# Performance work log

Measured on AMD Instinct MI355X. Metric: run time of the kernel, lower is better.

The kernel has to match this reference:

```python
import jax, jax.numpy as jnp
import numpy as np
from jax import lax


def get_grid(h, w):
    # normalized [-1,1] grid, channel 0 = x, channel 1 = y, shape [1,h,w,2]
    gx, gy = jnp.meshgrid(jnp.linspace(-1.0, 1.0, w), jnp.linspace(-1.0, 1.0, h))
    return jnp.stack([gx, gy], axis=-1)[None].astype(jnp.float32)


def gaussian_kernel(k, sigma=1.0):
    c = jnp.arange(k, dtype=jnp.float32) - (k - 1) / 2.0
    g = jnp.exp(-(c ** 2) / (2.0 * sigma ** 2))
    k2 = jnp.outer(g, g)
    return k2 / k2.sum()


def resize_bilinear(x, H, W):
    # x: [B,C,h,w]; torch F.interpolate(mode='bilinear', align_corners=False)
    B, C, h, w = x.shape
    def coords(n_out, n_in):
        c = (jnp.arange(n_out, dtype=jnp.float32) + 0.5) * (n_in / n_out) - 0.5
        c = jnp.clip(c, 0.0, n_in - 1.0)
        lo = jnp.floor(c).astype(jnp.int32)
        hi = jnp.minimum(lo + 1, n_in - 1)
        return lo, hi, c - lo.astype(jnp.float32)
    y0, y1, wy = coords(H, h)
    x0, x1, wx = coords(W, w)
    r = x[:, :, y0, :] * (1.0 - wy)[None, None, :, None] + x[:, :, y1, :] * wy[None, None, :, None]
    return r[:, :, :, x0] * (1.0 - wx) + r[:, :, :, x1] * wx


def _forward(src_grid, kernel, src_grid_base, tgt_grid, niter):
    B = src_grid.shape[0]
    H, W = tgt_grid.shape[1], tgt_grid.shape[2]
    ks = kernel.shape[-1]
    HW = H * W
    # forward displacement, resampled to target resolution, in pixel units
    dsrc = (src_grid - src_grid_base).transpose(0, 3, 1, 2)        # [B,2,Hs,Ws]
    dsrc = resize_bilinear(dsrc, H, W)                              # [B,2,H,W]
    dx = dsrc[:, 0].reshape(B, HW) * (W / 2.0)
    dy = dsrc[:, 1].reshape(B, HW) * (H / 2.0)
    xg = (jnp.arange(HW) % W).astype(jnp.float32)
    yg = (jnp.arange(HW) // W).astype(jnp.float32)
    xi = jnp.round(xg[None] + dx).astype(jnp.int32)
    yi = jnp.round(yg[None] + dy).astype(jnp.int32)
    oob = (xi < 0) | (yi < 0) | (xi > W - 1) | (yi > H - 1)
    field = jnp.where(oob, -1, yi * W + xi) + 1   # index 0 = trash slot
    # sort + dedup: duplicates are redirected to the trash slot
    order = jnp.argsort(field, axis=1)            # stable
    sf = jnp.take_along_axis(field, order, axis=1)
    keep = jnp.concatenate([jnp.ones((B, 1), bool), sf[:, 1:] != sf[:, :-1]], axis=1)
    sf = sf * keep
    inv_order = jnp.argsort(order, axis=1)
    field = jnp.take_along_axis(sf, inv_order, axis=1)
    # scatter inverse displacement (unique indices except trash slot 0)
    z = jnp.zeros((B, 1), dtype=dx.dtype)
    dxp = jnp.concatenate([z, dx], axis=1)
    dyp = jnp.concatenate([z, dy], axis=1)
    fieldp = jnp.concatenate([jnp.zeros((B, 1), field.dtype), field], axis=1)
    bidx = jnp.arange(B)[:, None]
    inv_dx = jnp.zeros_like(dxp).at[bidx, fieldp].set(-dxp)[:, 1:].reshape(B, H, W)
    inv_dy = jnp.zeros_like(dyp).at[bidx, fieldp].set(-dyp)[:, 1:].reshape(B, H, W)
    mask = (jnp.zeros_like(dxp).at[bidx, fieldp].set(1.0)[:, 1:].reshape(B, H, W)) > 0.5
    # pad so hole-fill never reads outside
    p = niter + 1
    inv_dx = jnp.pad(inv_dx, ((0, 0), (p, p), (p, p)))
    inv_dy = jnp.pad(inv_dy, ((0, 0), (p, p), (p, p)))
    mask = jnp.pad(mask, ((0, 0), (p, p), (p, p)))
    pd = ks // 2
    k4 = kernel.reshape(1, 1, ks, ks)
    def conv(x):
        return lax.conv_general_dilated(x[:, None], k4, (1, 1), [(pd, pd), (pd, pd)])[:, 0]
    # hole-fill: dilate mask by 4-neighborhood, fill with gaussian-weighted avg
    for _ in range(niter):
        nb = (jnp.pad(mask, ((0, 0), (1, 0), (0, 0)))[:, :-1]
              | jnp.pad(mask, ((0, 0), (0, 1), (0, 0)))[:, 1:]
              | jnp.pad(mask, ((0, 0), (0, 0), (1, 0)))[:, :, :-1]
              | jnp.pad(mask, ((0, 0), (0, 0), (0, 1)))[:, :, 1:])
        new_mask = (~mask) & nb
        new_dx = conv(inv_dx)
        new_dy = conv(inv_dy)
        new_sum = conv(mask.astype(inv_dx.dtype))
        denom = jnp.where(new_mask, new_sum, 1.0)  # safe: new_sum>0 where new_mask
        inv_dx = jnp.where(new_mask, new_dx / denom, inv_dx)
        inv_dy = jnp.where(new_mask, new_dy / denom, inv_dy)
        mask = mask | new_mask
    # erode: drop pixels with any unmasked 4-neighbor (outside counts as masked)
    for _ in range(niter):
        full = (jnp.pad(mask, ((0, 0), (1, 0), (0, 0)), constant_values=True)[:, :-1]
                & jnp.pad(mask, ((0, 0), (0, 1), (0, 0)), constant_values=True)[:, 1:]
                & jnp.pad(mask, ((0, 0), (0, 0), (1, 0)), constant_values=True)[:, :, :-1]
                & jnp.pad(mask, ((0, 0), (0, 0), (0, 1)), constant_values=True)[:, :, 1:])
        mask = mask & full
    inv_dx = jnp.where(mask, inv_dx, 2.0 * W)
    inv_dy = jnp.where(mask, inv_dy, 2.0 * H)
    inv_dx = inv_dx[:, p:-p, p:-p]
    inv_dy = inv_dy[:, p:-p, p:-p]
    dtgt = jnp.stack([inv_dx * (2.0 / W), inv_dy * (2.0 / H)], axis=3)
    return tgt_grid + dtgt


def setup_inputs() -> dict:
    key = jax.random.key(0)
    B, Hs, Ws, H, W = 8, 256, 256, 512, 512
    base = get_grid(Hs, Ws)
    src_grid = base + 0.05 * jax.random.normal(key, (B, Hs, Ws, 2), jnp.float32)
    return {
        "src_grid": src_grid,
        "kernel": gaussian_kernel(3),
        "src_grid_base": base,
        "tgt_grid": get_grid(H, W),
        "niter": 5,
    }


def reference(src_grid, kernel, src_grid_base, tgt_grid, niter):
    return _forward(src_grid, kernel, src_grid_base, tgt_grid, niter)
```

## Files before the change

### kernel.cpp

```cpp
#include <hip/hip_runtime.h>
#include <hip/hip_fp16.h>

typedef unsigned long long u64;
typedef unsigned int u32;
typedef float float4a __attribute__((ext_vector_type(4), aligned(4)));

#define B_    8
#define HS_   256
#define WS_   256
#define H_    512
#define W_    512
#define HW_   (H_ * W_)
#define TO_Y  16
#define WR    36
#define WCOLS 276
#define VR    26
#define VCOLS 266
#define VSTR  267
#define OW    9
#define NBAND 32
#define NBKT  64
#define INFW  0xFFFFFFFFu
#define CAPB  8192

__device__ __forceinline__ void bilin_disp(const float* __restrict__ src,
                                           const float* __restrict__ base,
                                           int b, int y, int x,
                                           float& dx, float& dy) {
#pragma clang fp contract(off)
    float cy = ((float)y + 0.5f) * 0.5f - 0.5f;
    cy = fminf(fmaxf(cy, 0.0f), 255.0f);
    int   y0 = (int)floorf(cy);
    int   y1 = min(y0 + 1, HS_ - 1);
    float wy = cy - (float)y0;

    float cx = ((float)x + 0.5f) * 0.5f - 0.5f;
    cx = fminf(fmaxf(cx, 0.0f), 255.0f);
    int   x0 = (int)floorf(cx);
    float wx = cx - (float)x0;

    float omy = 1.0f - wy;
    float wA, wB;
    int xs;
    if (x0 >= WS_ - 1) { xs = WS_ - 2; wA = 0.0f; wB = 1.0f; }
    else               { xs = x0;      wA = 1.0f - wx; wB = wx; }

    const float4a* S0 = (const float4a*)(src  + ((b * HS_ + y0) * WS_ + xs) * 2);
    const float4a* S1 = (const float4a*)(src  + ((b * HS_ + y1) * WS_ + xs) * 2);
    const float4a* B0 = (const float4a*)(base + (y0 * WS_ + xs) * 2);
    const float4a* B1 = (const float4a*)(base + (y1 * WS_ + xs) * 2);
    float4a s0 = *S0, s1 = *S1, b0 = *B0, b1 = *B1;

    float a00x = s0.x - b0.x, a00y = s0.y - b0.y;
    float a01x = s0.z - b0.z, a01y = s0.w - b0.w;
    float a10x = s1.x - b1.x, a10y = s1.y - b1.y;
    float a11x = s1.z - b1.z, a11y = s1.w - b1.w;

    float r0x = a00x * omy + a10x * wy;
    float r0y = a00y * omy + a10y * wy;
    float r1x = a01x * omy + a11x * wy;
    float r1y = a01y * omy + a11y * wy;
    dx = (r0x * wA + r1x * wB) * 256.0f;
    dy = (r0y * wA + r1y * wB) * 256.0f;
}

__device__ __forceinline__ u32 pack16(float x, float y) {
    __half hx = __float2half_rn(x), hy = __float2half_rn(y);
    return ((u32)__half_as_ushort(hy) << 16) | (u32)__half_as_ushort(hx);
}
__device__ __forceinline__ float2 unpack16(u32 p) {
    float2 f;
    f.x = __half2float(__ushort_as_half((unsigned short)(p & 0xFFFFu)));
    f.y = __half2float(__ushort_as_half((unsigned short)(p >> 16)));
    return f;
}

__device__ __forceinline__ u64 shfl_left(u64 v) {
    unsigned lo = __shfl_up((unsigned)v, 1);
    unsigned hi = __shfl_up((unsigned)(v >> 32), 1);
    u64 r = ((u64)hi << 32) | lo;
    return (threadIdx.x & 63) ? r : 0ull;
}
__device__ __forceinline__ u64 shfl_right(u64 v) {
    unsigned lo = __shfl_down((unsigned)v, 1);
    unsigned hi = __shfl_down((unsigned)(v >> 32), 1);
    u64 r = ((u64)hi << 32) | lo;
    return ((threadIdx.x & 63) == 63) ? 0ull : r;
}

__launch_bounds__(1024)
__global__ void pre_k(const float* __restrict__ src,
                      const float* __restrict__ base,
                      u32* __restrict__ pay,
                      u32* __restrict__ gcount,
                      u32* __restrict__ bucket) {
    __shared__ u32 cnt[NBKT];
    __shared__ u32 bbase[NBKT];

    int bid = blockIdx.x;
    int b   = bid & 7;
    int t   = bid >> 3;
    int j   = t * 1024 + threadIdx.x;
    int y   = j >> 9;
    int x   = j & (W_ - 1);

    if (threadIdx.x < NBKT) cnt[threadIdx.x] = 0;
    __syncthreads();

    float dx, dy;
    bilin_disp(src, base, b, y, x, dx, dy);
    pay[b * HW_ + j] = pack16(-dx, -dy);

    int xi = (int)rintf((float)x + dx);
    int yi = (int)rintf((float)y + dy);
    bool inb = (xi >= 0 && xi < W_ && yi >= 0 && yi < H_);
    int bk0 = 0, bk1 = -1;
    u32 r0 = 0, r1 = 0, e = 0;
    if (inb) {
        int band = yi >> 4;
        bk0 = band * 2 + (xi >> 8);
        r0 = atomicAdd(&cnt[bk0], 1u);
        if      (xi >= 246 && xi <= 255) bk1 = band * 2 + 1;
        else if (xi >= 256 && xi <= 265) bk1 = band * 2;
        if (bk1 >= 0) r1 = atomicAdd(&cnt[bk1], 1u);
        e = ((u32)(yi & 15) << 27) | ((u32)xi << 18) | (u32)j;
    }
    __syncthreads();
    if (threadIdx.x < NBKT) {
        u32 c = cnt[threadIdx.x];
        bbase[threadIdx.x] = c ? atomicAdd(&gcount[b * NBKT + threadIdx.x], c)
                               : 0u;
    }
    __syncthreads();
    if (inb) {
        u32 s0 = bbase[bk0] + r0;
        if (s0 < CAPB) bucket[(b * NBKT + bk0) * CAPB + s0] = e;
        if (bk1 >= 0) {
            u32 s1 = bbase[bk1] + r1;
            if (s1 < CAPB) bucket[(b * NBKT + bk1) * CAPB + s1] = e;
        }
    }
}

__launch_bounds__(512, 2)
__global__ void fused5_k(const u32* __restrict__ pay,
                         const u32* __restrict__ gcount,
                         const u32* __restrict__ bucket,
                         const float* __restrict__ kern,
                         const float* __restrict__ tgt,
                         float* __restrict__ out) {
    __shared__ u32 plane[VR * VSTR + WR * OW];
    u32* occ = plane + VR * VSTR;

    int id   = blockIdx.x;
    int b    = id & 7;
    int rest = id >> 3;
    int tile = rest >> 1;
    int half = rest & 1;
    int X0   = half << 8;
    int Y0   = tile * TO_Y;
    int w0   = Y0 - 10;
    int wc0  = X0 - 10;
    int tid  = threadIdx.x;

    float kw[9];
#pragma unroll
    for (int q = 0; q < 9; q++) kw[q] = kern[q];

    for (int i = tid; i < VR * VSTR; i += 512) plane[i] = INFW;
    for (int i = tid; i < WR * OW; i += 512) occ[i] = 0u;
    __syncthreads();

    {
        int qlo = max(0, w0 >> 4);
        int qhi = min(NBAND - 1, (w0 + WR - 1) >> 4);
        for (int q = qlo; q <= qhi; q++) {
            int bki = b * NBKT + q * 2 + half;
            u32 cntq = min(gcount[bki], (u32)CAPB);
            const u32* bk = bucket + bki * CAPB;
            int ybase = q * 16 - w0;
            for (u32 i = tid; i < cntq; i += 512) {
                u32 e  = bk[i];
                int wr = ybase + (int)((e >> 27) & 15u);
                if ((unsigned)wr < WR) {
                    int xc = (int)((e >> 18) & 511u) - wc0;
                    atomicOr(&occ[wr * OW + (xc >> 5)], 1u << (xc & 31));
                    unsigned vr = (unsigned)(wr - 5);
                    unsigned vc = (unsigned)(xc - 5);
                    if (vr < (unsigned)VR && vc < (unsigned)VCOLS)
                        atomicMin(&plane[vr * VSTR + vc], e & 0x3FFFFu);
                }
            }
        }
    }
    __syncthreads();

    int wv   = tid >> 6;
    int lane = tid & 63;
    int col  = X0 + 32 * wv - 16 + lane;
    int cls  = col - wc0;
    int clsv = cls - 5;
    bool colin = ((unsigned)cls < WCOLS)
                 && (col >= -6) && (col <= W_ + 5);

    u64 m = 0;
    if (colin) {
        int wsh = cls & 31, wix = cls >> 5;
#pragma unroll 6
        for (int r = 0; r < WR; r++)
            m |= (u64)((occ[r * OW + wix] >> wsh) & 1u) << r;
    }

    {
        const u32* pb = pay + b * HW_;
        for (int idx = tid; idx < VR * VCOLS; idx += 512) {
            int rr = idx / VCOLS;
            int cc = idx - rr * VCOLS;
            int off = rr * VSTR + cc;
            u32 k = plane[off];
            plane[off] = (k != INFW) ? pb[k] : 0u;
        }
    }
    __syncthreads();

    int rlo = max(0, -6 - w0);
    int rhi = min(WR - 1, (W_ + 5) - w0);
    u64 validm = colin ? ((((u64)1 << (rhi - rlo + 1)) - 1) << rlo) : 0ull;

    const u64 VROWS = (((u64)1 << 24) - 1) << 6;
    bool vupd = (lane >= 6 && lane <= 57)
                && (col >= X0 - 4) && (col <= X0 + 259);

    for (int it = 0; it < 5; it++) {
        u64 mL = shfl_left(m), mR = shfl_right(m);
        u64 cand = ~m & ((m << 1) | (m >> 1) | mL | mR) & validm;
        u64 cv = vupd ? (cand & VROWS) : 0ull;
        while (cv) {
            int r = __builtin_ctzll(cv);
            cv &= cv - 1;
            int rv = r - 5;
            float s = 0.0f, ax = 0.0f, ay = 0.0f;
#pragma unroll
            for (int dr = -1; dr <= 1; dr++) {
#pragma unroll
                for (int dc = -1; dc <= 1; dc++) {
                    if (dr == 0 && dc == 0) continue;
                    u64 nm = (dc < 0) ? mL : ((dc > 0) ? mR : m);
                    float wq = ((nm >> (r + dr)) & 1)
                                 ? kw[(dr + 1) * 3 + (dc + 1)] : 0.0f;
                    int cc = min(max(clsv + dc, 0), VCOLS - 1);
                    float2 nv = unpack16(plane[(rv + dr) * VSTR + cc]);
                    s += wq; ax += wq * nv.x; ay += wq * nv.y;
                }
            }
            float rs = __builtin_amdgcn_rcpf(s);
            plane[rv * VSTR + clsv] = pack16(ax * rs, ay * rs);
        }
        m |= cand;
        __syncthreads();
    }

    for (int it = 0; it < 5; it++) {
        u64 mL = shfl_left(m), mR = shfl_right(m);
        m &= (m << 1) & (m >> 1) & mL & mR;
    }

    if (lane >= 16 && lane < 48) {
#pragma unroll 4
        for (int r = 10; r < 10 + TO_Y; r++) {
            int row = w0 + r;
            bool on = (m >> r) & 1;
            float vx, vy;
            if (on) {
                float2 t = unpack16(plane[(r - 5) * VSTR + clsv]);
                vx = t.x * (1.0f / 256.0f);
                vy = t.y * (1.0f / 256.0f);
            } else {
                vx = 4.0f; vy = 4.0f;
            }
            int ti = (row * W_ + col) * 2;
            float2 tg = *(const float2*)(tgt + ti);
            float2 ov; ov.x = tg.x + vx; ov.y = tg.y + vy;
            ((float2*)out)[(size_t)b * HW_ + row * W_ + col] = ov;
        }
    }
}

extern "C" void kernel_launch(void* const* d_in, const int* in_sizes, int n_in,
                              void* d_out, int out_size, void* d_ws, size_t ws_size,
                              hipStream_t stream) {
    const float* src  = (const float*)d_in[0];
    const float* kern = (const float*)d_in[1];
    const float* base = (const float*)d_in[2];
    const float* tgt  = (const float*)d_in[3];
    float* out = (float*)d_out;

    char* ws = (char*)d_ws;
    u32* gcount = (u32*)ws;
    u32* pay    = (u32*)(ws + 4096);
    u32* bucket = (u32*)(ws + 4096 + (size_t)B_ * HW_ * 4);

    hipMemsetAsync(gcount, 0, B_ * NBKT * sizeof(u32), stream);

    pre_k<<<(B_ * HW_) / 1024, 1024, 0, stream>>>(src, base, pay, gcount, bucket);
    fused5_k<<<512, 512, 0, stream>>>(pay, gcount, bucket, kern, tgt, out);
}
```

Baseline: 139.2 us.

## Keep inpainting column in registers and exchange neighbors via wave shuffles

```diff
diff --git a/kernel.cpp b/kernel.cpp
--- a/kernel.cpp
+++ b/kernel.cpp
@@ -223,6 +223,14 @@
     }
     __syncthreads();
 
+    u32 v[VR];
+    {
+        int ccl = min(max(clsv, 0), VCOLS - 1);
+#pragma unroll
+        for (int rv = 0; rv < VR; ++rv)
+            v[rv] = plane[rv * VSTR + ccl];
+    }
+
     int rlo = max(0, -6 - w0);
     int rhi = min(WR - 1, (W_ + 5) - w0);
     u64 validm = colin ? ((((u64)1 << (rhi - rlo + 1)) - 1) << rlo) : 0ull;
@@ -231,34 +239,45 @@
     bool vupd = (lane >= 6 && lane <= 57)
                 && (col >= X0 - 4) && (col <= X0 + 259);
 
+#define TAP(val, on, w)                                         \
+    {                                                           \
+        float wq = (on) ? (w) : 0.0f;                           \
+        float2 f_ = unpack16(val);                              \
+        s += wq; ax += wq * f_.x; ay += wq * f_.y;              \
+    }
+#pragma unroll 1
     for (int it = 0; it < 5; it++) {
         u64 mL = shfl_left(m), mR = shfl_right(m);
         u64 cand = ~m & ((m << 1) | (m >> 1) | mL | mR) & validm;
         u64 cv = vupd ? (cand & VROWS) : 0ull;
-        while (cv) {
-            int r = __builtin_ctzll(cv);
-            cv &= cv - 1;
-            int rv = r - 5;
-            float s = 0.0f, ax = 0.0f, ay = 0.0f;
 #pragma unroll
-            for (int dr = -1; dr <= 1; dr++) {
-#pragma unroll
-                for (int dc = -1; dc <= 1; dc++) {
-                    if (dr == 0 && dc == 0) continue;
-                    u64 nm = (dc < 0) ? mL : ((dc > 0) ? mR : m);
-                    float wq = ((nm >> (r + dr)) & 1)
-                                 ? kw[(dr + 1) * 3 + (dc + 1)] : 0.0f;
-                    int cc = min(max(clsv + dc, 0), VCOLS - 1);
-                    float2 nv = unpack16(plane[(rv + dr) * VSTR + cc]);
-                    s += wq; ax += wq * nv.x; ay += wq * nv.y;
-                }
+        for (int r = 6; r <= 29; ++r) {
+            if (__any((int)((cv >> r) & 1))) {
+                const int rv = r - 5;
+                u32 cm = v[rv - 1], cp = v[rv + 1];
+                u32 lm = __shfl_up(v[rv - 1], 1);
+                u32 l0 = __shfl_up(v[rv],     1);
+                u32 lp = __shfl_up(v[rv + 1], 1);
+                u32 rm = __shfl_down(v[rv - 1], 1);
+                u32 r0 = __shfl_down(v[rv],     1);
+                u32 rp = __shfl_down(v[rv + 1], 1);
+                float s = 0.0f, ax = 0.0f, ay = 0.0f;
+                TAP(cm, (m  >> (r - 1)) & 1, kw[1]);
+                TAP(cp, (m  >> (r + 1)) & 1, kw[7]);
+                TAP(lm, (mL >> (r - 1)) & 1, kw[0]);
+                TAP(l0, (mL >>  r     ) & 1, kw[3]);
+                TAP(lp, (mL >> (r + 1)) & 1, kw[6]);
+                TAP(rm, (mR >> (r - 1)) & 1, kw[2]);
+                TAP(r0, (mR >>  r     ) & 1, kw[5]);
+                TAP(rp, (mR >> (r + 1)) & 1, kw[8]);
+                float rs = __builtin_amdgcn_rcpf(s);
+                u32 nv = pack16(ax * rs, ay * rs);
+                if ((cv >> r) & 1) v[rv] = nv;
             }
-            float rs = __builtin_amdgcn_rcpf(s);
-            plane[rv * VSTR + clsv] = pack16(ax * rs, ay * rs);
         }
         m |= cand;
-        __syncthreads();
-    }
+    }
+#undef TAP
 
     for (int it = 0; it < 5; it++) {
         u64 mL = shfl_left(m), mR = shfl_right(m);
@@ -266,13 +285,13 @@
     }
 
     if (lane >= 16 && lane < 48) {
-#pragma unroll 4
+#pragma unroll
         for (int r = 10; r < 10 + TO_Y; r++) {
             int row = w0 + r;
             bool on = (m >> r) & 1;
             float vx, vy;
             if (on) {
-                float2 t = unpack16(plane[(r - 5) * VSTR + clsv]);
+                float2 t = unpack16(v[r - 5]);
                 vx = t.x * (1.0f / 256.0f);
                 vy = t.y * (1.0f / 256.0f);
             } else {
```

New measurement: 141.5 us. About the same (+1.6%).
